# Performance work log

Hardware: AMD Instinct MI355X
Metric: run time of the kernel (lower is better)

The kernel has to match this reference:

```python
import jax, jax.numpy as jnp
import numpy as np

N = 10000      # nodes per graph
E = 160000     # random edges per graph (plus N self-loops)
IN_DIM = 4096
HID = 64       # num_hidden
H = 8          # heads
C = 5          # num_classes
SLOPE = 0.2    # LeakyReLU negative slope


def gat_conv(x, src, dst, W, al, ar, b, res_W=None):
    """DGL-style GATConv. x:(N,F) -> (N,H,D). Messages flow src->dst,
    edge softmax over in-edges of each dst node."""
    n = x.shape[0]
    h, d = al.shape
    feat = (x @ W).reshape(n, h, d)                      # (N,H,D)
    el = jnp.sum(feat * al, axis=-1)                     # (N,H)
    er = jnp.sum(feat * ar, axis=-1)                     # (N,H)
    e = jax.nn.leaky_relu(el[src] + er[dst], SLOPE)      # (E,H)
    emax = jax.ops.segment_max(e, dst, num_segments=n)   # (N,H) stable softmax
    ex = jnp.exp(e - emax[dst])
    denom = jax.ops.segment_sum(ex, dst, num_segments=n)
    alpha = ex / denom[dst]                              # (E,H)
    out = jax.ops.segment_sum(feat[src] * alpha[..., None], dst, num_segments=n)
    if res_W is not None:
        out = out + (x @ res_W).reshape(n, h, d)         # residual projection
    return out + b.reshape(h, d)


def encoder(x, src, dst, W0, al0, ar0, b0, W1, al1, ar1, b1):
    h0 = jax.nn.elu(gat_conv(x, src, dst, W0, al0, ar0, b0))   # (N,H,D)
    h0 = h0.reshape(h0.shape[0], -1)                           # flatten(1)
    return jax.nn.elu(gat_conv(h0, src, dst, W1, al1, ar1, b1))


def setup_inputs() -> dict:
    key = jax.random.key(0)
    ks = list(jax.random.split(key, 40))
    ki = iter(ks)

    def edges(k):
        k1, k2 = jax.random.split(k)
        loop = jnp.arange(N, dtype=jnp.int32)
        s = jnp.concatenate([jax.random.randint(k1, (E,), 0, N, dtype=jnp.int32), loop])
        d = jnp.concatenate([jax.random.randint(k2, (E,), 0, N, dtype=jnp.int32), loop])
        return s, d

    inp = {}
    for name in ("s0", "s1", "t"):
        s, d = edges(next(ki))
        inp[f"src_{name}"], inp[f"dst_{name}"] = s, d
    inp["features_s0"] = jax.random.normal(next(ki), (N, IN_DIM), jnp.float32)
    inp["features_s1"] = jax.random.normal(next(ki), (N, IN_DIM), jnp.float32)
    inp["features_t"]  = jax.random.normal(next(ki), (N, IN_DIM), jnp.float32)

    def lin(k, fan_in, fan_out):
        return jax.random.normal(k, (fan_in, fan_out), jnp.float32) / np.sqrt(fan_in)

    inp["W0"] = lin(next(ki), IN_DIM, H * HID)
    inp["al0"] = 0.1 * jax.random.normal(next(ki), (H, HID), jnp.float32)
    inp["ar0"] = 0.1 * jax.random.normal(next(ki), (H, HID), jnp.float32)
    inp["b0"] = jnp.zeros((H * HID,), jnp.float32)
    inp["W1"] = lin(next(ki), H * HID, H * HID)
    inp["al1"] = 0.1 * jax.random.normal(next(ki), (H, HID), jnp.float32)
    inp["ar1"] = 0.1 * jax.random.normal(next(ki), (H, HID), jnp.float32)
    inp["b1"] = jnp.zeros((H * HID,), jnp.float32)
    for k_idx in (0, 1):
        inp[f"Wc{k_idx}"] = lin(next(ki), H * HID, H * C)
        inp[f"alc{k_idx}"] = 0.1 * jax.random.normal(next(ki), (H, C), jnp.float32)
        inp[f"arc{k_idx}"] = 0.1 * jax.random.normal(next(ki), (H, C), jnp.float32)
        inp[f"bc{k_idx}"] = jnp.zeros((H * C,), jnp.float32)
        inp[f"rW{k_idx}"] = lin(next(ki), H * HID, H * C)
    inp["num_source"] = 2
    return inp


def reference(features_s0, features_s1, features_t,
              W0, al0, ar0, b0, W1, al1, ar1, b1,
              Wc0, alc0, arc0, bc0, rW0,
              Wc1, alc1, arc1, bc1, rW1,
              src_s0, dst_s0, src_s1, dst_s1, src_t, dst_t,
              num_source):
    enc_p = (W0, al0, ar0, b0, W1, al1, ar1, b1)
    cls_p = [(Wc0, alc0, arc0, bc0, rW0), (Wc1, alc1, arc1, bc1, rW1)]
    feats = [features_s0, features_s1]
    graphs = [(src_s0, dst_s0), (src_s1, dst_s1)]

    # shared-weight encoder on each source graph
    h_s = [encoder(feats[i], graphs[i][0], graphs[i][1], *enc_p)
           for i in range(num_source)]                    # each (N,H,HID)
    # per-source classifiers on their own graphs, mean over heads
    pred_s = []
    for i in range(num_source):
        Wc, alc, arc, bc, rW = cls_p[i]
        s, d = graphs[i]
        logits = gat_conv(h_s[i].reshape(N, -1), s, d, Wc, alc, arc, bc, res_W=rW)
        pred_s.append(logits.mean(axis=1))               # (N,C)
    emb_s = [h.reshape(N, -1) for h in h_s]

    # target: every source classifier applied to the target graph
    h_t = encoder(features_t, src_t, dst_t, *enc_p)
    pred_t = []
    for i in range(num_source):
        Wc, alc, arc, bc, rW = cls_p[i]
        logits = gat_conv(h_t.reshape(N, -1), src_t, dst_t, Wc, alc, arc, bc, res_W=rW)
        pred_t.append(logits.mean(axis=1))
    emb_t = h_t.reshape(N, -1)

    return (pred_s[0], pred_s[1], pred_t[0], pred_t[1], emb_s[0], emb_s[1], emb_t)
```

## Files before the change

### kernel.cpp

```cpp
#include <hip/hip_runtime.h>
#include <stdint.h>

typedef _Float16 f16;
typedef _Float16 f16x2 __attribute__((ext_vector_type(2)));
typedef _Float16 f16x8 __attribute__((ext_vector_type(8)));
typedef float f32x4 __attribute__((ext_vector_type(4)));

#define AS1 __attribute__((address_space(1)))
#define AS3 __attribute__((address_space(3)))

#define NN 10000
#define NP 10112
#define KK0 4096
#define FF 512

__global__ void k_count_b(const int* __restrict__ d0, const int* __restrict__ d1,
                          const int* __restrict__ d2, int E0, int E1, int E2,
                          int nb0, int nb1, int* __restrict__ deg){
  int b = blockIdx.x;
  const int* d; int Eg, base, lb;
  if (b < nb0){ d=d0; Eg=E0; base=0; lb=b; }
  else if (b < nb0+nb1){ d=d1; Eg=E1; base=NN; lb=b-nb0; }
  else { d=d2; Eg=E2; base=2*NN; lb=b-nb0-nb1; }
  int i = lb*256 + threadIdx.x;
  if (i < Eg) atomicAdd(&deg[base + d[i]], 1);
}

__global__ __launch_bounds__(1024) void k_scan_b(const int* __restrict__ deg_all,
    int* __restrict__ rowptr_all, int* __restrict__ cursor_all){
  int g = blockIdx.x;
  const int* deg = deg_all + g*NN;
  int* rowptr = rowptr_all + g*(NN+1);
  int* cursor = cursor_all + g*NN;
  __shared__ int ps[1024];
  int t = threadIdx.x;
  const int CH = 16;
  int i0 = t*CH;
  int sum = 0;
  for (int k=0;k<CH;k++){ int i=i0+k; if (i<NN) sum += deg[i]; }
  ps[t]=sum; __syncthreads();
  for (int off=1; off<1024; off<<=1){
    int v = (t>=off)? ps[t-off] : 0;
    __syncthreads();
    ps[t] += v;
    __syncthreads();
  }
  int run = ps[t]-sum;
  for (int k=0;k<CH;k++){
    int i=i0+k;
    if (i<=NN) rowptr[i]=run;
    if (i<NN){ cursor[i]=run; run += deg[i]; }
  }
}

__global__ void k_fill_b(const int* __restrict__ s0, const int* __restrict__ d0,
                         const int* __restrict__ s1, const int* __restrict__ d1,
                         const int* __restrict__ s2, const int* __restrict__ d2,
                         int E0, int E1, int E2, int nb0, int nb1,
                         int* __restrict__ cursor_all,
                         int* __restrict__ c0, int* __restrict__ c1, int* __restrict__ c2){
  int b = blockIdx.x;
  const int *s, *d; int Eg, lb; int* cur; int* col;
  if (b < nb0){ s=s0; d=d0; Eg=E0; lb=b; cur=cursor_all; col=c0; }
  else if (b < nb0+nb1){ s=s1; d=d1; Eg=E1; lb=b-nb0; cur=cursor_all+NN; col=c1; }
  else { s=s2; d=d2; Eg=E2; lb=b-nb0-nb1; cur=cursor_all+2*NN; col=c2; }
  int i = lb*256 + threadIdx.x;
  if (i >= Eg) return;
  int slot = atomicAdd(&cur[d[i]], 1);
  col[slot] = s[i];
}

__global__ void k_transpose_t(const float* __restrict__ W, f16* __restrict__ WT,
                              int K, int Nc){
  __shared__ float tile[32][33];
  int n0 = blockIdx.x*32, k0 = blockIdx.y*32;
  int tx = threadIdx.x, ty = threadIdx.y;
  #pragma unroll
  for (int i=0;i<32;i+=8)
    tile[ty+i][tx] = W[(long)(k0+ty+i)*Nc + n0+tx];
  __syncthreads();
  #pragma unroll
  for (int i=0;i<32;i+=8)
    WT[(long)(n0+ty+i)*K + k0+tx] = (f16)tile[tx][ty+i];
}

__global__ void k_pack_wc(const float* __restrict__ Wc, const float* __restrict__ rW,
                          f16* __restrict__ WT){
  int idx = blockIdx.x*256 + threadIdx.x;
  if (idx >= 128*512) return;
  int n = idx >> 9; int k = idx & 511;
  float v = 0.f;
  if (n < 40) v = Wc[k*40 + n];
  else if (n < 80) v = rW[k*40 + (n-40)];
  WT[idx] = (f16)v;
}

template<bool CVT>
__global__ __launch_bounds__(512,1) void k_gemmw(
    const void* __restrict__ A0v, const void* __restrict__ A1v, const void* __restrict__ A2v,
    f16* __restrict__ C0, f16* __restrict__ C1, f16* __restrict__ C2,
    const f16* __restrict__ B,
    const float* __restrict__ alp, const float* __restrict__ arp,
    float* __restrict__ elp, float* __restrict__ erp)
{
  constexpr int K = CVT ? KK0 : FF;
  constexpr int nt = K >> 6;
  __shared__ f16 lds[2][40960];

  const int nwg = gridDim.x;
  const int qd = nwg>>3, rd = nwg&7;
  const int xcd = blockIdx.x & 7, bx = blockIdx.x >> 3;
  const int wid = (xcd < rd ? xcd*(qd+1) : rd*(qd+1) + (xcd-rd)*qd) + bx;
  const int task = wid / 79;
  const int tr = wid - task*79;

  f16* C = task==0?C0:(task==1?C1:C2);

  const int t = threadIdx.x;
  const int wave = t >> 6, lane = t & 63;
  const int slot = (lane&7) ^ (lane>>3);
  const int arow0 = t >> 3;
  const int ak8 = t & 7;

  #define GLDSB(kt, buf) { \
    int ko = (kt)*64; \
    _Pragma("unroll") \
    for (int i=0;i<8;i++){ \
      int br = i*64 + wave*8 + (lane>>3); \
      __builtin_amdgcn_global_load_lds((const AS1 void*)(B + (long)br*K + ko + slot*8), \
          (AS3 void*)(&lds[buf][8192 + i*4096 + wave*512]), 16, 0, 0); \
    } }

  int abyte[2][8], bbyte[2][4];
  #pragma unroll
  for (int ks=0;ks<2;ks++){
    #pragma unroll
    for (int m=0;m<8;m++){
      int row = m*16 + (lane&15);
      abyte[ks][m] = row*128 + (((ks*4 + (lane>>4))*16) ^ ((row&7)<<4));
    }
    #pragma unroll
    for (int n=0;n<4;n++){
      int brow = wave*64 + n*16 + (lane&15);
      bbyte[ks][n] = 16384 + brow*128 + (((ks*4 + (lane>>4))*16) ^ ((brow&7)<<4));
    }
  }

  f32x4 zero4 = {0.f,0.f,0.f,0.f};
  f32x4 acc[8][4];
  #pragma unroll
  for (int m=0;m<8;m++)
    #pragma unroll
    for (int n=0;n<4;n++) acc[m][n] = zero4;

  #define MFMA_TILE(buf) { \
    const char* Ls = (const char*)&lds[buf][0]; \
    _Pragma("unroll") \
    for (int ks=0;ks<2;ks++){ \
      f16x8 bf[4]; \
      _Pragma("unroll") \
      for (int n=0;n<4;n++) bf[n] = *(const f16x8*)(Ls + bbyte[ks][n]); \
      _Pragma("unroll") \
      for (int m=0;m<8;m++){ \
        f16x8 af = *(const f16x8*)(Ls + abyte[ks][m]); \
        _Pragma("unroll") \
        for (int n=0;n<4;n++) \
          acc[m][n] = __builtin_amdgcn_mfma_f32_16x16x32_f16(af, bf[n], acc[m][n], 0, 0, 0); \
      } \
    } }

  int cur = 0;
  if constexpr (CVT){
    const float* Af = task==0?(const float*)A0v:(task==1?(const float*)A1v:(const float*)A2v);
    const float* gA[2];
    bool okA[2];
    #pragma unroll
    for (int s=0;s<2;s++){
      int grow = tr*128 + arow0 + s*64;
      okA[s] = grow < NN;
      gA[s] = Af + (long)(okA[s] ? grow : 0)*KK0 + ak8*8;
    }
    f32x4 arE[2][2];

    #define LOADA(kt) { \
      _Pragma("unroll") \
      for (int s=0;s<2;s++){ \
        arE[s][0] = *(const f32x4*)(gA[s] + (kt)*64); \
        arE[s][1] = *(const f32x4*)(gA[s] + (kt)*64 + 4); \
      } }
    #define WRITEA(buf) { \
      _Pragma("unroll") \
      for (int s=0;s<2;s++){ \
        int row = arow0 + s*64; \
        f16x8 v; \
        _Pragma("unroll") \
        for (int j=0;j<4;j++){ \
          v[j]   = okA[s] ? (f16)arE[s][0][j] : (f16)0.f; \
          v[4+j] = okA[s] ? (f16)arE[s][1][j] : (f16)0.f; \
        } \
        *(f16x8*)(&lds[buf][row*64 + ((ak8 ^ (arow0&7))*8)]) = v; \
      } }

    LOADA(0);
    __builtin_amdgcn_sched_barrier(0);
    GLDSB(0, 0);
    __builtin_amdgcn_sched_barrier(0);
    WRITEA(0);
    __builtin_amdgcn_sched_barrier(0);
    LOADA(1);
    __builtin_amdgcn_sched_barrier(0);
    asm volatile("s_waitcnt vmcnt(4) lgkmcnt(0)" ::: "memory");
    __builtin_amdgcn_s_barrier();

    for (int kt=0; kt<nt; kt++){
      if (kt+1 < nt){
        WRITEA(cur^1);
        __builtin_amdgcn_sched_barrier(0);
        GLDSB(kt+1, cur^1);
        __builtin_amdgcn_sched_barrier(0);
      }
      if (kt+2 < nt){
        LOADA(kt+2);
        __builtin_amdgcn_sched_barrier(0);
      }
      MFMA_TILE(cur);
      if (kt+1 < nt){
        __builtin_amdgcn_sched_barrier(0);
        if (kt+2 < nt)
          asm volatile("s_waitcnt vmcnt(4) lgkmcnt(0)" ::: "memory");
        else
          asm volatile("s_waitcnt vmcnt(0) lgkmcnt(0)" ::: "memory");
        __builtin_amdgcn_s_barrier();
      }
      cur ^= 1;
    }
    #undef LOADA
    #undef WRITEA
  } else {
    const f16* Ah = task==0?(const f16*)A0v:(task==1?(const f16*)A1v:(const f16*)A2v);
    const f16* Ab = Ah + (long)tr*128*K;
    const int r8 = lane>>3;

    #define GLDSA(kt, buf) { \
      _Pragma("unroll") \
      for (int s=0;s<2;s++){ \
        int arow = wave*8 + r8 + s*64; \
        __builtin_amdgcn_global_load_lds((const AS1 void*)(Ab + (long)arow*K + (kt)*64 + slot*8), \
            (AS3 void*)(&lds[buf][s*4096 + wave*512]), 16, 0, 0); \
      } }

    GLDSA(0, 0);
    GLDSB(0, 0);
    __syncthreads();
    for (int kt=0; kt<nt; kt++){
      if (kt+1 < nt){
        GLDSA(kt+1, cur^1);
        GLDSB(kt+1, cur^1);
      }
      MFMA_TILE(cur);
      __syncthreads();
      cur ^= 1;
    }
    #undef GLDSA
  }
  #undef GLDSB
  #undef MFMA_TILE

  #pragma unroll
  for (int m=0;m<8;m++){
    int row0 = tr*128 + m*16 + ((lane>>4)<<2);
    #pragma unroll
    for (int n=0;n<4;n++){
      int col = wave*64 + n*16 + (lane&15);
      #pragma unroll
      for (int q2=0;q2<4;q2++)
        C[(long)(row0+q2)*FF + col] = (f16)acc[m][n][q2];
    }
  }

  {
    const int head = wave;
    const float* alh = alp + head*64;
    const float* arh = arp + head*64;
    float alv[4], arv[4];
    #pragma unroll
    for (int n=0;n<4;n++){ int d = n*16 + (lane&15); alv[n]=alh[d]; arv[n]=arh[d]; }
    float* elo = elp + (long)task*NN*8;
    float* ero = erp + (long)task*NN*8;
    #pragma unroll
    for (int m=0;m<8;m++){
      float e0,e1,e2,e3,r0,r1,r2,r3;
      #pragma unroll
      for (int qq=0;qq<4;qq++){
        float e=0.f, rr=0.f;
        #pragma unroll
        for (int n=0;n<4;n++){ e += acc[m][n][qq]*alv[n]; rr += acc[m][n][qq]*arv[n]; }
        #pragma unroll
        for (int off=1; off<16; off<<=1){ e += __shfl_xor(e, off); rr += __shfl_xor(rr, off); }
        if (qq==0){e0=e;r0=rr;} else if (qq==1){e1=e;r1=rr;} else if (qq==2){e2=e;r2=rr;} else {e3=e;r3=rr;}
      }
      int qq = lane&15;
      if (qq < 4){
        int node = tr*128 + m*16 + ((lane>>4)<<2) + qq;
        if (node < NN){
          float ev = qq==0?e0:(qq==1?e1:(qq==2?e2:e3));
          float rv = qq==0?r0:(qq==1?r1:(qq==2?r2:r3));
          long o = (long)node*8 + head;
          elo[o] = ev;
          ero[o] = rv;
        }
      }
    }
  }
}

struct GemmTasks { const f16* A[4]; const f16* B[4]; f16* C[4]; };

__global__ __launch_bounds__(256,3) void k_gemmb(GemmTasks p, int ntpb, int ntn,
                                                 int Nc, int K){
  __shared__ f16 lds[2][12288];
  const int bid = blockIdx.x;
  const int task = bid / ntpb;
  const int orig = bid - task*ntpb;
  const int q = ntpb >> 3, r = ntpb & 7;
  const int xcd = orig & 7, bx = orig >> 3;
  const int wid = (xcd < r ? xcd*(q+1) : r*(q+1) + (xcd-r)*q) + bx;
  const int tr = wid / ntn, tc = wid - tr*ntn;

  const f16* A = p.A[task];
  const f16* B = p.B[task];
  f16* C = p.C[task];

  const int t = threadIdx.x;
  const int wave = t >> 6, lane = t & 63;
  const int wr = wave >> 1, wc = wave & 1;

  const f16* Ab = A + (long)tr*64*K;
  const f16* Bb = B + (long)tc*128*K;

  const int slot = (lane&7) ^ (lane>>3);
  const int rbase = wave*8 + (lane>>3);

  f32x4 zero4 = {0.f,0.f,0.f,0.f};
  f32x4 acc[2][4];
  #pragma unroll
  for (int m=0;m<2;m++)
    #pragma unroll
    for (int n=0;n<4;n++) acc[m][n] = zero4;

  int abyte[2][2], bbyte[2][4];
  #pragma unroll
  for (int ks=0;ks<2;ks++){
    #pragma unroll
    for (int m=0;m<2;m++){
      int row = wr*32 + m*16 + (lane&15);
      abyte[ks][m] = row*128 + (((ks*4 + (lane>>4))*16) ^ ((row&7)<<4));
    }
    #pragma unroll
    for (int n=0;n<4;n++){
      int brow = wc*64 + n*16 + (lane&15);
      bbyte[ks][n] = 8192 + brow*128 + (((ks*4 + (lane>>4))*16) ^ ((brow&7)<<4));
    }
  }

  const int nt = K >> 6;
  int cur = 0;

  #pragma unroll
  for (int i=0;i<2;i++)
    __builtin_amdgcn_global_load_lds((const AS1 void*)(Ab + (i*32+rbase)*K + slot*8),
        (AS3 void*)(&lds[0][i*2048 + wave*512]), 16, 0, 0);
  #pragma unroll
  for (int i=0;i<4;i++)
    __builtin_amdgcn_global_load_lds((const AS1 void*)(Bb + (i*32+rbase)*K + slot*8),
        (AS3 void*)(&lds[0][4096 + i*2048 + wave*512]), 16, 0, 0);
  __syncthreads();

  for (int kt=0; kt<nt; kt++){
    if (kt+1 < nt){
      int ko = (kt+1)<<6;
      #pragma unroll
      for (int i=0;i<2;i++)
        __builtin_amdgcn_global_load_lds((const AS1 void*)(Ab + ko + (i*32+rbase)*K + slot*8),
            (AS3 void*)(&lds[cur^1][i*2048 + wave*512]), 16, 0, 0);
      #pragma unroll
      for (int i=0;i<4;i++)
        __builtin_amdgcn_global_load_lds((const AS1 void*)(Bb + ko + (i*32+rbase)*K + slot*8),
            (AS3 void*)(&lds[cur^1][4096 + i*2048 + wave*512]), 16, 0, 0);
    }
    const char* Ls = (const char*)&lds[cur][0];
    #pragma unroll
    for (int ks=0;ks<2;ks++){
      f16x8 af[2], bf[4];
      #pragma unroll
      for (int m=0;m<2;m++) af[m] = *(const f16x8*)(Ls + abyte[ks][m]);
      #pragma unroll
      for (int n=0;n<4;n++) bf[n] = *(const f16x8*)(Ls + bbyte[ks][n]);
      #pragma unroll
      for (int m=0;m<2;m++)
        #pragma unroll
        for (int n=0;n<4;n++)
          acc[m][n] = __builtin_amdgcn_mfma_f32_16x16x32_f16(af[m], bf[n], acc[m][n], 0, 0, 0);
    }
    __syncthreads();
    cur ^= 1;
  }

  #pragma unroll
  for (int m=0;m<2;m++){
    int row0 = tr*64 + wr*32 + m*16 + ((lane>>4)<<2);
    #pragma unroll
    for (int n=0;n<4;n++){
      int col = tc*128 + wc*64 + n*16 + (lane&15);
      #pragma unroll
      for (int q2=0;q2<4;q2++)
        C[(long)(row0+q2)*Nc + col] = (f16)acc[m][n][q2];
    }
  }
}

#define MAXD 128

struct AggArgs {
  const int* rp[3]; const int* cs[3];
  const float* el; const float* er;
  const f16* feat[3];
  const float* bias;
  f16* outH[3];
  float* outF[3];
};

__global__ __launch_bounds__(256) void k_agg_b(AggArgs a){
  int b = blockIdx.x;
  int g = b / NN, n = b - g*NN;
  const int* rowptr = a.rp[g];
  const int* colsrc = a.cs[g];
  const float* el = a.el + (long)g*NN*8;
  const f16* featH = a.feat[g];
  int t = threadIdx.x;
  __shared__ float sm[MAXD*8];
  __shared__ int   scol[MAXD];
  __shared__ float red[256];
  __shared__ float inv[8];
  __shared__ float ern[8];
  if (t < 8) ern[t] = a.er[((long)g*NN+n)*8+t];
  __syncthreads();
  int j0 = rowptr[n], deg = rowptr[n+1]-j0;
  int h2 = t >> 5;
  int c = t*2;
  float a0=0.f, a1=0.f;

  if (deg <= MAXD){
    {
      int h = t & 7;
      float dsum = 0.f;
      for (int jj = t>>3; jj < deg; jj += 32){
        int s = colsrc[j0+jj];
        float v = el[s*8+h] + ern[h];
        v = (v>0.f)? v : 0.2f*v;
        float ex = __expf(v);
        dsum += ex;
        sm[jj*8+h] = ex;
        if (h==0) scol[jj] = s;
      }
      red[t] = dsum; __syncthreads();
      if (t<128) red[t] += red[t+128]; __syncthreads();
      if (t<64)  red[t] += red[t+64];  __syncthreads();
      if (t<32)  red[t] += red[t+32];  __syncthreads();
      if (t<16)  red[t] += red[t+16];  __syncthreads();
      if (t<8)   inv[t] = 1.0f / (red[t] + red[t+8]);
      __syncthreads();
    }
    float ivh = inv[h2];
    int jj = 0;
    for (; jj+4<=deg; jj+=4){
      int s0=scol[jj], s1=scol[jj+1], s2=scol[jj+2], s3=scol[jj+3];
      float x0=sm[(jj+0)*8+h2], x1=sm[(jj+1)*8+h2], x2=sm[(jj+2)*8+h2], x3=sm[(jj+3)*8+h2];
      f16x2 f0 = *(const f16x2*)(featH + (long)s0*FF + c);
      f16x2 f1 = *(const f16x2*)(featH + (long)s1*FF + c);
      f16x2 f2 = *(const f16x2*)(featH + (long)s2*FF + c);
      f16x2 f3 = *(const f16x2*)(featH + (long)s3*FF + c);
      a0 += x0*(float)f0[0] + x1*(float)f1[0] + x2*(float)f2[0] + x3*(float)f3[0];
      a1 += x0*(float)f0[1] + x1*(float)f1[1] + x2*(float)f2[1] + x3*(float)f3[1];
    }
    for (; jj<deg; jj++){
      int s = scol[jj];
      float x = sm[jj*8+h2];
      f16x2 f = *(const f16x2*)(featH + (long)s*FF + c);
      a0 += x*(float)f[0];
      a1 += x*(float)f[1];
    }
    a0 *= ivh; a1 *= ivh;
  } else {
    {
      int h = t & 7;
      float dsum = 0.f;
      for (int jj = t>>3; jj < deg; jj += 32){
        int s = colsrc[j0+jj];
        float v = el[s*8+h] + ern[h];
        v = (v>0.f)? v : 0.2f*v;
        float ex = __expf(v);
        dsum += ex;
        if (jj < MAXD){
          sm[jj*8+h] = ex;
          if (h==0) scol[jj] = s;
        }
      }
      red[t] = dsum; __syncthreads();
      if (t<128) red[t] += red[t+128]; __syncthreads();
      if (t<64)  red[t] += red[t+64];  __syncthreads();
      if (t<32)  red[t] += red[t+32];  __syncthreads();
      if (t<16)  red[t] += red[t+16];  __syncthreads();
      if (t<8)   inv[t] = 1.0f / (red[t] + red[t+8]);
      __syncthreads();
    }
    float ivh = inv[h2];
    for (int jj=0; jj<deg; jj++){
      int s; float ex;
      if (jj < MAXD){ s = scol[jj]; ex = sm[jj*8+h2]; }
      else {
        s = colsrc[j0+jj];
        float v = el[s*8+h2] + ern[h2];
        v = (v>0.f)? v : 0.2f*v;
        ex = __expf(v);
      }
      float alpha = ex * ivh;
      f16x2 f = *(const f16x2*)(featH + (long)s*FF + c);
      a0 += alpha*(float)f[0];
      a1 += alpha*(float)f[1];
    }
  }

  a0 += a.bias[c]; a1 += a.bias[c+1];
  a0 = (a0>0.f)? a0 : __expf(a0)-1.f;
  a1 = (a1>0.f)? a1 : __expf(a1)-1.f;
  f16x2 o; o[0]=(f16)a0; o[1]=(f16)a1;
  *(f16x2*)(a.outH[g] + (long)n*FF + c) = o;
  float* oF = a.outF[g];
  if (oF){
    oF[(long)n*FF + c]     = a0;
    oF[(long)n*FF + c + 1] = a1;
  }
}

__global__ void k_elerc_b(const f16* __restrict__ fc,
    const float* __restrict__ alc0, const float* __restrict__ arc0,
    const float* __restrict__ alc1, const float* __restrict__ arc1,
    float* __restrict__ el, float* __restrict__ er){
  int idx = blockIdx.x*256 + threadIdx.x;
  if (idx >= 4*NN*8) return;
  int ti = idx / (NN*8);
  int rem = idx - ti*NN*8;
  int n = rem>>3, hh = rem&7;
  const f16* featc = fc + (long)ti*NP*128;
  const float* al = (ti&1) ? alc1 : alc0;
  const float* ar_ = (ti&1) ? arc1 : arc0;
  float a=0.f, bsum=0.f;
  #pragma unroll
  for (int cc=0; cc<5; cc++){
    float v = (float)featc[(long)n*128 + hh*5 + cc];
    a += v*al[hh*5+cc];
    bsum += v*ar_[hh*5+cc];
  }
  el[idx]=a; er[idx]=bsum;
}

struct ClsArgs {
  const int* rp[3]; const int* cs[3];
  const float* el; const float* er;
  const f16* fc;
  const float* bc[2];
  float* pred;
};

__global__ __launch_bounds__(64) void k_cls_b(ClsArgs a){
  int b = blockIdx.x;
  int ti = b / NN, n = b - ti*NN;
  int g = ti<2 ? ti : 2;
  int ci = ti&1;
  const int* rowptr = a.rp[g];
  const int* colsrc = a.cs[g];
  const float* el = a.el + (long)ti*NN*8;
  const f16* featc = a.fc + (long)ti*NP*128;
  const float* bc = a.bc[ci];
  float* pred = a.pred + (long)ti*5*NN;
  int l = threadIdx.x;
  __shared__ float sm[MAXD*8];
  __shared__ int   scol[MAXD];
  __shared__ float inv[8];
  __shared__ float ern[8];
  __shared__ float lg[40];
  if (l<8) ern[l] = a.er[((long)ti*NN+n)*8+l];
  __syncthreads();
  int j0 = rowptr[n], deg = rowptr[n+1]-j0;

  if (deg <= MAXD){
    {
      int h = l & 7;
      float dsum = 0.f;
      for (int jj = l>>3; jj < deg; jj += 8){
        int s = colsrc[j0+jj];
        float v = el[s*8+h] + ern[h];
        v = (v>0.f)? v : 0.2f*v;
        float ex = __expf(v);
        dsum += ex;
        sm[jj*8+h] = ex;
        if (h==0) scol[jj] = s;
      }
      dsum += __shfl_xor(dsum, 8);
      dsum += __shfl_xor(dsum, 16);
      dsum += __shfl_xor(dsum, 32);
      if (l<8) inv[l] = 1.0f/dsum;
    }
    __syncthreads();
    if (l<40){
      int h = l/5;
      float ivh = inv[h];
      float acc = 0.f;
      int jj = 0;
      for (; jj+4<=deg; jj+=4){
        int s0=scol[jj], s1=scol[jj+1], s2=scol[jj+2], s3=scol[jj+3];
        float x0=sm[(jj+0)*8+h], x1=sm[(jj+1)*8+h], x2=sm[(jj+2)*8+h], x3=sm[(jj+3)*8+h];
        float v0=(float)featc[(long)s0*128 + l];
        float v1=(float)featc[(long)s1*128 + l];
        float v2=(float)featc[(long)s2*128 + l];
        float v3=(float)featc[(long)s3*128 + l];
        acc += x0*v0 + x1*v1 + x2*v2 + x3*v3;
      }
      for (; jj<deg; jj++)
        acc += sm[jj*8+h] * (float)featc[(long)scol[jj]*128 + l];
      acc *= ivh;
      acc += (float)featc[(long)n*128 + 40 + l];
      acc += bc[l];
      lg[l] = acc;
    }
  } else {
    {
      int h = l & 7;
      float dsum = 0.f;
      for (int jj = l>>3; jj < deg; jj += 8){
        int s = colsrc[j0+jj];
        float v = el[s*8+h] + ern[h];
        v = (v>0.f)? v : 0.2f*v;
        float ex = __expf(v);
        dsum += ex;
        if (jj < MAXD){
          sm[jj*8+h] = ex;
          if (h==0) scol[jj] = s;
        }
      }
      dsum += __shfl_xor(dsum, 8);
      dsum += __shfl_xor(dsum, 16);
      dsum += __shfl_xor(dsum, 32);
      if (l<8) inv[l] = 1.0f/dsum;
    }
    __syncthreads();
    if (l<40){
      int h = l/5;
      float ivh = inv[h];
      float acc = 0.f;
      for (int jj=0; jj<deg; jj++){
        int s; float ex;
        if (jj < MAXD){ s = scol[jj]; ex = sm[jj*8+h]; }
        else {
          s = colsrc[j0+jj];
          float v = el[s*8+h] + ern[h];
          v = (v>0.f)? v : 0.2f*v;
          ex = __expf(v);
        }
        acc += ex*ivh * (float)featc[(long)s*128 + l];
      }
      acc += (float)featc[(long)n*128 + 40 + l];
      acc += bc[l];
      lg[l] = acc;
    }
  }
  __syncthreads();
  if (l<5){
    float p=0.f;
    #pragma unroll
    for (int h=0;h<8;h++) p += lg[h*5+l];
    pred[(long)n*5 + l] = p*0.125f;
  }
}

extern "C" void kernel_launch(void* const* d_in, const int* in_sizes, int n_in,
                              void* d_out, int out_size, void* d_ws, size_t ws_size,
                              hipStream_t stream){
  const int* srcs[3] = {(const int*)d_in[0], (const int*)d_in[2], (const int*)d_in[4]};
  const int* dsts[3] = {(const int*)d_in[1], (const int*)d_in[3], (const int*)d_in[5]};
  int E[3] = {in_sizes[0], in_sizes[2], in_sizes[4]};
  const float* X[3] = {(const float*)d_in[6], (const float*)d_in[7], (const float*)d_in[8]};
  const float* W0  = (const float*)d_in[9];
  const float* al0 = (const float*)d_in[10];
  const float* ar0 = (const float*)d_in[11];
  const float* b0  = (const float*)d_in[12];
  const float* W1  = (const float*)d_in[13];
  const float* al1 = (const float*)d_in[14];
  const float* ar1 = (const float*)d_in[15];
  const float* b1  = (const float*)d_in[16];
  const float* Wcv[2] = {(const float*)d_in[17], (const float*)d_in[22]};
  const float* alc[2] = {(const float*)d_in[18], (const float*)d_in[23]};
  const float* arc[2] = {(const float*)d_in[19], (const float*)d_in[24]};
  const float* bcv[2] = {(const float*)d_in[20], (const float*)d_in[25]};
  const float* rWv[2] = {(const float*)d_in[21], (const float*)d_in[26]};

  float* out = (float*)d_out;
  float* embOut[3] = {out+200000, out+200000+(long)NN*FF, out+200000+2L*NN*FF};

  char* w = (char*)d_ws;
  size_t off = 0;
  auto alloc = [&](size_t bytes)->void*{
    void* p = (void*)(w + off);
    off += (bytes + 255) & ~((size_t)255);
    return p;
  };
  f16* W0T = (f16*)alloc((size_t)FF*KK0*2);
  f16* W1T = (f16*)alloc((size_t)FF*FF*2);
  f16* WcT[2] = {(f16*)alloc(128*512*2), (f16*)alloc(128*512*2)};
  f16* feat0H[3], *h0H[3], *feat1H[3], *embH[3];
  for (int g=0;g<3;g++) feat0H[g] = (f16*)alloc((size_t)NP*FF*2);
  for (int g=0;g<3;g++) h0H[g]    = (f16*)alloc((size_t)NP*FF*2);
  for (int g=0;g<3;g++) feat1H[g] = (f16*)alloc((size_t)NP*FF*2);
  for (int g=0;g<3;g++) embH[g]   = (f16*)alloc((size_t)NP*FF*2);
  f16* featc = (f16*)alloc((size_t)4*NP*128*2);
  float* el_e = (float*)alloc((size_t)3*NN*8*4);
  float* er_e = (float*)alloc((size_t)3*NN*8*4);
  float* el_c = (float*)alloc((size_t)4*NN*8*4);
  float* er_c = (float*)alloc((size_t)4*NN*8*4);
  int* deg    = (int*)alloc((size_t)3*NN*4);
  int* cursor = (int*)alloc((size_t)3*NN*4);
  int* rowptr = (int*)alloc((size_t)3*(NN+1)*4);
  int* colsrc[3];
  for (int g=0;g<3;g++) colsrc[g] = (int*)alloc((size_t)E[g]*4);
  (void)ws_size; (void)n_in; (void)out_size;

  int nb[3] = {(E[0]+255)/256, (E[1]+255)/256, (E[2]+255)/256};
  hipMemsetAsync(deg, 0, (size_t)3*NN*4, stream);
  k_count_b<<<nb[0]+nb[1]+nb[2], 256, 0, stream>>>(dsts[0], dsts[1], dsts[2],
      E[0], E[1], E[2], nb[0], nb[1], deg);
  k_scan_b<<<3, 1024, 0, stream>>>(deg, rowptr, cursor);
  k_fill_b<<<nb[0]+nb[1]+nb[2], 256, 0, stream>>>(srcs[0], dsts[0], srcs[1], dsts[1],
      srcs[2], dsts[2], E[0], E[1], E[2], nb[0], nb[1], cursor,
      colsrc[0], colsrc[1], colsrc[2]);

  k_transpose_t<<<dim3(FF/32, KK0/32), dim3(32,8), 0, stream>>>(W0, W0T, KK0, FF);
  k_transpose_t<<<dim3(FF/32, FF/32), dim3(32,8), 0, stream>>>(W1, W1T, FF, FF);
  k_pack_wc<<<(128*512+255)/256, 256, 0, stream>>>(Wcv[0], rWv[0], WcT[0]);
  k_pack_wc<<<(128*512+255)/256, 256, 0, stream>>>(Wcv[1], rWv[1], WcT[1]);

  const int* rp[3] = {rowptr, rowptr+(NN+1), rowptr+2*(NN+1)};

  k_gemmw<true><<<237, 512, 0, stream>>>(X[0], X[1], X[2],
      feat0H[0], feat0H[1], feat0H[2], W0T, al0, ar0, el_e, er_e);
  {
    AggArgs a;
    for (int g=0;g<3;g++){ a.rp[g]=rp[g]; a.cs[g]=colsrc[g]; a.feat[g]=feat0H[g];
                           a.outH[g]=h0H[g]; a.outF[g]=nullptr; }
    a.el = el_e; a.er = er_e; a.bias = b0;
    k_agg_b<<<3*NN, 256, 0, stream>>>(a);
  }

  k_gemmw<false><<<237, 512, 0, stream>>>(h0H[0], h0H[1], h0H[2],
      feat1H[0], feat1H[1], feat1H[2], W1T, al1, ar1, el_e, er_e);
  {
    AggArgs a;
    for (int g=0;g<3;g++){ a.rp[g]=rp[g]; a.cs[g]=colsrc[g]; a.feat[g]=feat1H[g];
                           a.outH[g]=embH[g]; a.outF[g]=embOut[g]; }
    a.el = el_e; a.er = er_e; a.bias = b1;
    k_agg_b<<<3*NN, 256, 0, stream>>>(a);
  }

  {
    GemmTasks p;
    const int tg[4] = {0,1,2,2};
    for (int i=0;i<4;i++){ p.A[i]=embH[tg[i]]; p.B[i]=WcT[i&1]; p.C[i]=featc + (long)i*NP*128; }
    k_gemmb<<<4*158, 256, 0, stream>>>(p, 158, 1, 128, FF);
  }
  k_elerc_b<<<(4*NN*8+255)/256, 256, 0, stream>>>(featc, alc[0], arc[0], alc[1], arc[1], el_c, er_c);
  {
    ClsArgs a;
    for (int g=0;g<3;g++){ a.rp[g]=rp[g]; a.cs[g]=colsrc[g]; }
    a.el = el_c; a.er = er_c; a.fc = featc;
    a.bc[0] = bcv[0]; a.bc[1] = bcv[1];
    a.pred = out;
    k_cls_b<<<4*NN, 64, 0, stream>>>(a);
  }
}
```

Baseline: 500.6 us.

## Split first-layer GEMM into smaller 64x256 tiles with higher occupancy

The first-layer fp32-input GEMM (K=4096) moves from 128x512 tiles at one block per CU (237 blocks) to 64x256 tiles with launch_bounds(512,4) (948 blocks) and half the LDS per block. The aim is better load balance across the CUs and more waves in flight to hide global-load latency on the fp32 A stream. The el/er head reductions are now combined across two waves through LDS because each head spans two waves. In exchange, each X row is read twice (once per column tile), arithmetic intensity per tile is lower, and the hand-tuned two-deep prefetch with explicit waitcnt is replaced by a simpler single-stage prefetch.

```diff
diff --git a/kernel.cpp b/kernel.cpp
--- a/kernel.cpp
+++ b/kernel.cpp
@@ -95,15 +95,181 @@
   WT[idx] = (f16)v;
 }
 
-template<bool CVT>
-__global__ __launch_bounds__(512,1) void k_gemmw(
-    const void* __restrict__ A0v, const void* __restrict__ A1v, const void* __restrict__ A2v,
+__global__ __launch_bounds__(512,4) void k_gemm0s(
+    const float* __restrict__ X0, const float* __restrict__ X1, const float* __restrict__ X2,
     f16* __restrict__ C0, f16* __restrict__ C1, f16* __restrict__ C2,
     const f16* __restrict__ B,
     const float* __restrict__ alp, const float* __restrict__ arp,
     float* __restrict__ elp, float* __restrict__ erp)
 {
-  constexpr int K = CVT ? KK0 : FF;
+  constexpr int K = KK0;
+  constexpr int nt = K >> 6;
+  __shared__ f16 lds[2][20480];
+
+  const int nwg = gridDim.x;
+  const int qd = nwg>>3, rd = nwg&7;
+  const int xcd = blockIdx.x & 7, bx = blockIdx.x >> 3;
+  const int wid = (xcd < rd ? xcd*(qd+1) : rd*(qd+1) + (xcd-rd)*qd) + bx;
+  const int task = wid / 316;
+  const int rem = wid - task*316;
+  const int tr = rem >> 1, tc = rem & 1;
+
+  const float* A = task==0 ? X0 : (task==1 ? X1 : X2);
+  f16* C = task==0 ? C0 : (task==1 ? C1 : C2);
+  const f16* Bb = B + (long)tc*256*K;
+
+  const int t = threadIdx.x;
+  const int wave = t >> 6, lane = t & 63;
+  const int slot = (lane&7) ^ (lane>>3);
+
+  const int arow = t >> 3;
+  const int ak8 = t & 7;
+  const bool okA = (tr*64 + arow) < NN;
+  const float* gA = A + (long)(okA ? tr*64+arow : 0)*KK0 + ak8*8;
+  f32x4 arE0, arE1;
+
+  #define LOADA(kt) { arE0 = *(const f32x4*)(gA + (kt)*64); \
+                      arE1 = *(const f32x4*)(gA + (kt)*64 + 4); }
+  #define WRITEA(buf) { \
+    f16x8 v; \
+    _Pragma("unroll") \
+    for (int j=0;j<4;j++){ \
+      v[j]   = okA ? (f16)arE0[j] : (f16)0.f; \
+      v[4+j] = okA ? (f16)arE1[j] : (f16)0.f; \
+    } \
+    *(f16x8*)(&lds[buf][arow*64 + ((ak8 ^ (arow&7))*8)]) = v; }
+
+  #define GLDSB(kt, buf) { \
+    _Pragma("unroll") \
+    for (int i=0;i<4;i++){ \
+      int br8 = i*8 + wave; \
+      __builtin_amdgcn_global_load_lds((const AS1 void*)(Bb + (long)(br8*8 + (lane>>3))*K + (kt)*64 + slot*8), \
+          (AS3 void*)(&lds[buf][4096 + br8*512]), 16, 0, 0); \
+    } }
+
+  int abyte[2][4], bbyte[2][2];
+  #pragma unroll
+  for (int ks=0;ks<2;ks++){
+    #pragma unroll
+    for (int m=0;m<4;m++){
+      int row = m*16 + (lane&15);
+      abyte[ks][m] = row*128 + (((ks*4 + (lane>>4))*16) ^ ((row&7)<<4));
+    }
+    #pragma unroll
+    for (int n=0;n<2;n++){
+      int brow = wave*32 + n*16 + (lane&15);
+      bbyte[ks][n] = 8192 + brow*128 + (((ks*4 + (lane>>4))*16) ^ ((brow&7)<<4));
+    }
+  }
+
+  f32x4 zero4 = {0.f,0.f,0.f,0.f};
+  f32x4 acc[4][2];
+  #pragma unroll
+  for (int m=0;m<4;m++)
+    #pragma unroll
+    for (int n=0;n<2;n++) acc[m][n] = zero4;
+
+  #define MFMA_TILE(buf) { \
+    const char* Ls = (const char*)&lds[buf][0]; \
+    _Pragma("unroll") \
+    for (int ks=0;ks<2;ks++){ \
+      f16x8 bf[2]; \
+      _Pragma("unroll") \
+      for (int n=0;n<2;n++) bf[n] = *(const f16x8*)(Ls + bbyte[ks][n]); \
+      _Pragma("unroll") \
+      for (int m=0;m<4;m++){ \
+        f16x8 af = *(const f16x8*)(Ls + abyte[ks][m]); \
+        _Pragma("unroll") \
+        for (int n=0;n<2;n++) \
+          acc[m][n] = __builtin_amdgcn_mfma_f32_16x16x32_f16(af, bf[n], acc[m][n], 0, 0, 0); \
+      } \
+    } }
+
+  LOADA(0);
+  GLDSB(0, 0);
+  WRITEA(0);
+  __syncthreads();
+
+  int cur = 0;
+  for (int kt=0; kt<nt; kt++){
+    if (kt+1 < nt){
+      LOADA(kt+1);
+      GLDSB(kt+1, cur^1);
+    }
+    MFMA_TILE(cur);
+    if (kt+1 < nt) WRITEA(cur^1);
+    __syncthreads();
+    cur ^= 1;
+  }
+  #undef LOADA
+  #undef WRITEA
+  #undef GLDSB
+  #undef MFMA_TILE
+
+  #pragma unroll
+  for (int m=0;m<4;m++){
+    int row0 = tr*64 + m*16 + ((lane>>4)<<2);
+    #pragma unroll
+    for (int n=0;n<2;n++){
+      int col = tc*256 + wave*32 + n*16 + (lane&15);
+      #pragma unroll
+      for (int q2=0;q2<4;q2++)
+        C[(long)(row0+q2)*FF + col] = (f16)acc[m][n][q2];
+    }
+  }
+
+  {
+    const int head = tc*4 + (wave>>1);
+    const float* alh = alp + head*64 + (wave&1)*32;
+    const float* arh = arp + head*64 + (wave&1)*32;
+    float alv[2], arv[2];
+    #pragma unroll
+    for (int n=0;n<2;n++){ int d = n*16 + (lane&15); alv[n]=alh[d]; arv[n]=arh[d]; }
+    float* pbuf = (float*)&lds[0][0];
+    #pragma unroll
+    for (int m=0;m<4;m++){
+      float e0,e1,e2,e3,r0,r1,r2,r3;
+      #pragma unroll
+      for (int qq=0;qq<4;qq++){
+        float e=0.f, rr=0.f;
+        #pragma unroll
+        for (int n=0;n<2;n++){ e += acc[m][n][qq]*alv[n]; rr += acc[m][n][qq]*arv[n]; }
+        #pragma unroll
+        for (int off=1; off<16; off<<=1){ e += __shfl_xor(e, off); rr += __shfl_xor(rr, off); }
+        if (qq==0){e0=e;r0=rr;} else if (qq==1){e1=e;r1=rr;} else if (qq==2){e2=e;r2=rr;} else {e3=e;r3=rr;}
+      }
+      int qq = lane&15;
+      if (qq < 4){
+        int row = m*16 + ((lane>>4)<<2) + qq;
+        float ev = qq==0?e0:(qq==1?e1:(qq==2?e2:e3));
+        float rv = qq==0?r0:(qq==1?r1:(qq==2?r2:r3));
+        pbuf[(wave*64 + row)*2]     = ev;
+        pbuf[(wave*64 + row)*2 + 1] = rv;
+      }
+    }
+    __syncthreads();
+    if ((wave&1)==0){
+      int node = tr*64 + lane;
+      if (node < NN){
+        float e = pbuf[(wave*64 + lane)*2]     + pbuf[((wave+1)*64 + lane)*2];
+        float r = pbuf[(wave*64 + lane)*2 + 1] + pbuf[((wave+1)*64 + lane)*2 + 1];
+        float* elo = elp + (long)task*NN*8;
+        float* ero = erp + (long)task*NN*8;
+        elo[(long)node*8 + head] = e;
+        ero[(long)node*8 + head] = r;
+      }
+    }
+  }
+}
+
+__global__ __launch_bounds__(512,1) void k_gemmw1(
+    const f16* __restrict__ A0, const f16* __restrict__ A1, const f16* __restrict__ A2,
+    f16* __restrict__ C0, f16* __restrict__ C1, f16* __restrict__ C2,
+    const f16* __restrict__ B,
+    const float* __restrict__ alp, const float* __restrict__ arp,
+    float* __restrict__ elp, float* __restrict__ erp)
+{
+  constexpr int K = FF;
   constexpr int nt = K >> 6;
   __shared__ f16 lds[2][40960];
 
@@ -114,13 +280,13 @@
   const int task = wid / 79;
   const int tr = wid - task*79;
 
+  const f16* Ah = task==0?A0:(task==1?A1:A2);
   f16* C = task==0?C0:(task==1?C1:C2);
 
   const int t = threadIdx.x;
   const int wave = t >> 6, lane = t & 63;
   const int slot = (lane&7) ^ (lane>>3);
-  const int arow0 = t >> 3;
-  const int ak8 = t & 7;
+  const int r8 = lane>>3;
 
   #define GLDSB(kt, buf) { \
     int ko = (kt)*64; \
@@ -129,6 +295,13 @@
       int br = i*64 + wave*8 + (lane>>3); \
       __builtin_amdgcn_global_load_lds((const AS1 void*)(B + (long)br*K + ko + slot*8), \
           (AS3 void*)(&lds[buf][8192 + i*4096 + wave*512]), 16, 0, 0); \
+    } }
+  #define GLDSA(kt, buf) { \
+    _Pragma("unroll") \
+    for (int s=0;s<2;s++){ \
+      int arow = wave*8 + r8 + s*64; \
+      __builtin_amdgcn_global_load_lds((const AS1 void*)(Ah + (long)tr*128*K + (long)arow*K + (kt)*64 + slot*8), \
+          (AS3 void*)(&lds[buf][s*4096 + wave*512]), 16, 0, 0); \
     } }
 
   int abyte[2][8], bbyte[2][4];
@@ -170,99 +343,19 @@
     } }
 
   int cur = 0;
-  if constexpr (CVT){
-    const float* Af = task==0?(const float*)A0v:(task==1?(const float*)A1v:(const float*)A2v);
-    const float* gA[2];
-    bool okA[2];
-    #pragma unroll
-    for (int s=0;s<2;s++){
-      int grow = tr*128 + arow0 + s*64;
-      okA[s] = grow < NN;
-      gA[s] = Af + (long)(okA[s] ? grow : 0)*KK0 + ak8*8;
-    }
-    f32x4 arE[2][2];
-
-    #define LOADA(kt) { \
-      _Pragma("unroll") \
-      for (int s=0;s<2;s++){ \
-        arE[s][0] = *(const f32x4*)(gA[s] + (kt)*64); \
-        arE[s][1] = *(const f32x4*)(gA[s] + (kt)*64 + 4); \
-      } }
-    #define WRITEA(buf) { \
-      _Pragma("unroll") \
-      for (int s=0;s<2;s++){ \
-        int row = arow0 + s*64; \
-        f16x8 v; \
-        _Pragma("unroll") \
-        for (int j=0;j<4;j++){ \
-          v[j]   = okA[s] ? (f16)arE[s][0][j] : (f16)0.f; \
-          v[4+j] = okA[s] ? (f16)arE[s][1][j] : (f16)0.f; \
-        } \
-        *(f16x8*)(&lds[buf][row*64 + ((ak8 ^ (arow0&7))*8)]) = v; \
-      } }
-
-    LOADA(0);
-    __builtin_amdgcn_sched_barrier(0);
-    GLDSB(0, 0);
-    __builtin_amdgcn_sched_barrier(0);
-    WRITEA(0);
-    __builtin_amdgcn_sched_barrier(0);
-    LOADA(1);
-    __builtin_amdgcn_sched_barrier(0);
-    asm volatile("s_waitcnt vmcnt(4) lgkmcnt(0)" ::: "memory");
-    __builtin_amdgcn_s_barrier();
-
-    for (int kt=0; kt<nt; kt++){
-      if (kt+1 < nt){
-        WRITEA(cur^1);
-        __builtin_amdgcn_sched_barrier(0);
-        GLDSB(kt+1, cur^1);
-        __builtin_amdgcn_sched_barrier(0);
-      }
-      if (kt+2 < nt){
-        LOADA(kt+2);
-        __builtin_amdgcn_sched_barrier(0);
-      }
-      MFMA_TILE(cur);
-      if (kt+1 < nt){
-        __builtin_amdgcn_sched_barrier(0);
-        if (kt+2 < nt)
-          asm volatile("s_waitcnt vmcnt(4) lgkmcnt(0)" ::: "memory");
-        else
-          asm volatile("s_waitcnt vmcnt(0) lgkmcnt(0)" ::: "memory");
-        __builtin_amdgcn_s_barrier();
-      }
-      cur ^= 1;
-    }
-    #undef LOADA
-    #undef WRITEA
-  } else {
-    const f16* Ah = task==0?(const f16*)A0v:(task==1?(const f16*)A1v:(const f16*)A2v);
-    const f16* Ab = Ah + (long)tr*128*K;
-    const int r8 = lane>>3;
-
-    #define GLDSA(kt, buf) { \
-      _Pragma("unroll") \
-      for (int s=0;s<2;s++){ \
-        int arow = wave*8 + r8 + s*64; \
-        __builtin_amdgcn_global_load_lds((const AS1 void*)(Ab + (long)arow*K + (kt)*64 + slot*8), \
-            (AS3 void*)(&lds[buf][s*4096 + wave*512]), 16, 0, 0); \
-      } }
-
-    GLDSA(0, 0);
-    GLDSB(0, 0);
+  GLDSA(0, 0);
+  GLDSB(0, 0);
+  __syncthreads();
+  for (int kt=0; kt<nt; kt++){
+    if (kt+1 < nt){
+      GLDSA(kt+1, cur^1);
+      GLDSB(kt+1, cur^1);
+    }
+    MFMA_TILE(cur);
     __syncthreads();
-    for (int kt=0; kt<nt; kt++){
-      if (kt+1 < nt){
-        GLDSA(kt+1, cur^1);
-        GLDSB(kt+1, cur^1);
-      }
-      MFMA_TILE(cur);
-      __syncthreads();
-      cur ^= 1;
-    }
-    #undef GLDSA
-  }
+    cur ^= 1;
+  }
+  #undef GLDSA
   #undef GLDSB
   #undef MFMA_TILE
 
@@ -751,7 +844,7 @@
 
   const int* rp[3] = {rowptr, rowptr+(NN+1), rowptr+2*(NN+1)};
 
-  k_gemmw<true><<<237, 512, 0, stream>>>(X[0], X[1], X[2],
+  k_gemm0s<<<948, 512, 0, stream>>>(X[0], X[1], X[2],
       feat0H[0], feat0H[1], feat0H[2], W0T, al0, ar0, el_e, er_e);
   {
     AggArgs a;
@@ -761,7 +854,7 @@
     k_agg_b<<<3*NN, 256, 0, stream>>>(a);
   }
 
-  k_gemmw<false><<<237, 512, 0, stream>>>(h0H[0], h0H[1], h0H[2],
+  k_gemmw1<<<237, 512, 0, stream>>>(h0H[0], h0H[1], h0H[2],
       feat1H[0], feat1H[1], feat1H[2], W1T, al1, ar1, el_e, er_e);
   {
     AggArgs a;
```

New measurement: 576.5 us. +15.2%, slower.
